# Optimization experiments

Measured on AMD Instinct MI355X. Metric: run time of the kernel, lower is better.

Reference implementation:

```python
import jax, jax.numpy as jnp
import numpy as np

X_DIM, R_DIM, U_DIM, V_DIM, H_DIM = 64, 64, 64, 64, 128


def setup_inputs() -> dict:
    key = jax.random.key(0)
    k1, k2, k3, k4, k5 = jax.random.split(key, 5)
    n, i, j = 8, 32, 32
    r = jax.random.normal(k1, (n, i, j, R_DIM), dtype=jnp.float32)
    u = jax.random.normal(k2, (n, R_DIM, U_DIM, V_DIM), dtype=jnp.float32)
    v = jax.random.normal(k3, (n, i, j, V_DIM), dtype=jnp.float32)
    # xavier_uniform scaling: gain=1, fan computed over last two dims per torch default
    def xavier(k, shape):
        fan_in, fan_out = shape[-1], shape[-2]
        # torch xavier on >2D tensor: fan_in = shape[1]*prod(shape[2:]), fan_out = shape[0]*prod(shape[2:])
        rf = int(np.prod(shape[2:])) if len(shape) > 2 else 1
        fi = shape[1] * rf
        fo = shape[0] * rf
        bound = float(np.sqrt(6.0 / (fi + fo)))
        return jax.random.uniform(k, shape, dtype=jnp.float32, minval=-bound, maxval=bound)
    w1 = xavier(k4, (R_DIM, U_DIM, V_DIM, H_DIM))
    w2 = xavier(k5, (X_DIM, R_DIM, H_DIM))
    return {"r": r, "u": u, "v": v, "w1": w1, "w2": w2}


def reference(r, u, v, w1, w2):
    # contract w1 with u over (u_dim, v_dim) -> per-batch tensor a[n, r, v', h]
    # original: einsum('ruvh,nruv,nijv->nijrh')
    a = jnp.einsum('ruvh,nruv->nrvh', w1, u)          # contract u axis; v survives? no:
    # Careful: in 'ruvh,nruv,nijv->nijrh', v is contracted across all three.
    # Do it in two GEMM-friendly steps: first contract u-axis, keeping v.
    # a: [n, r, v, h] (contracted only over u)
    a = jnp.einsum('ruvh,nruv->nrvh', w1, u)
    # then contract v with v-tensor: [n,i,j,v] x [n,r,v,h] -> [n,i,j,r,h]
    x = jax.nn.relu(jnp.einsum('nijv,nrvh->nijrh', v, a))
    # second einsum: 'xrh,nijr,nijrh->nijx'
    # fuse r-weighting into x first (elementwise over r), then contract (r,h) with w2
    out = jnp.einsum('xrh,nijrh->nijx', w2, x * r[..., None])
    return out
```

## Files before the change

### kernel.cpp

```cpp
#include <hip/hip_runtime.h>
#include <hip/hip_bf16.h>

#define RD 64
#define UD 64
#define VD 64
#define HD 128
#define XD 64
#define NB 8
#define SITES 1024

typedef float f32x4 __attribute__((ext_vector_type(4)));
typedef float f32x2 __attribute__((ext_vector_type(2)));
typedef __bf16 bf16x4 __attribute__((ext_vector_type(4)));
typedef __bf16 bf16x8 __attribute__((ext_vector_type(8)));
typedef unsigned int u32x4 __attribute__((ext_vector_type(4)));
typedef unsigned short u16;
typedef unsigned short u16x4 __attribute__((ext_vector_type(4)));

__device__ __forceinline__ void lds_barrier() {
  __builtin_amdgcn_s_waitcnt(0xC07F);
  __builtin_amdgcn_s_barrier();
}

__global__ void kprep(const float* __restrict__ w2, u16* __restrict__ w2t,
                      const float* __restrict__ r, float* __restrict__ rt,
                      const float* __restrict__ u, float* __restrict__ ut) {
  __shared__ float tl[64][68];
  int b = blockIdx.x;
  int t = threadIdx.x;
  if (b < 256) {
    int rr = b >> 2, qq = b & 3;
    for (int i = 0; i < 8; ++i) {
      int idx = qq * 2048 + i * 256 + t;
      int x = idx >> 7, h = idx & 127;
      float val = w2[((size_t)x * RD + rr) * HD + h];
      __hip_bfloat16 hv = __float2bfloat16(val);
      w2t[((size_t)rr * XD + x) * HD + h] = *(u16*)&hv;
    }
  } else if (b < 384) {
    int bb = b - 256;
    int n = bb >> 4, sb = (bb & 15) * 64;
    for (int i = 0; i < 4; ++i) {
      int flat = i * 256 + t;
      int s = flat >> 4, ch = flat & 15;
      f32x4 d = *(const f32x4*)(r + ((size_t)(n * SITES + sb + s) * RD + ch * 4));
      *(f32x4*)&tl[s][ch * 4] = d;
    }
    __syncthreads();
    for (int i = 0; i < 4; ++i) {
      int flat = i * 256 + t;
      int rr = flat >> 4, ch = flat & 15;
      f32x4 o;
      o.x = tl[ch * 4 + 0][rr];
      o.y = tl[ch * 4 + 1][rr];
      o.z = tl[ch * 4 + 2][rr];
      o.w = tl[ch * 4 + 3][rr];
      *(f32x4*)(rt + ((size_t)(n * RD + rr) * SITES + sb + ch * 4)) = o;
    }
  } else {
    int f = (b - 384) * 256 + t;
    int nh = f & 1, v = (f >> 1) & 63, uu = (f >> 7) & 63, rr = f >> 13;
    f32x4 o;
#pragma unroll
    for (int k = 0; k < 4; ++k)
      o[k] = u[(((size_t)(nh * 4 + k) * RD + rr) * UD + uu) * VD + v];
    *(f32x4*)(ut + (size_t)f * 4) = o;
  }
}

#define PF 8
__global__ __launch_bounds__(256, 1) void k_a_full(const float* __restrict__ w1,
                                                   const float* __restrict__ ut,
                                                   u16* __restrict__ at) {
  __shared__ float tile[8 * 128 * 17];
  int b = blockIdx.x;
  int rr = b >> 2, vq = b & 3;
  int t = threadIdx.x;
  int vl = t >> 4;
  int hs = t & 15;
  int v = vq * 16 + vl;
  int h0 = hs * 8;
  const float* w1p = w1 + ((size_t)rr * UD * VD + v) * HD + h0;
  const float* up  = ut + ((size_t)rr * UD * VD + v) * NB;

  f32x4 accA[8], accB[8];
#pragma unroll
  for (int n = 0; n < 8; ++n) { accA[n] = (f32x4)0.f; accB[n] = (f32x4)0.f; }

  f32x4 wa[PF], wb[PF], ua[PF], ub[PF];
#pragma unroll
  for (int p = 0; p < PF; ++p) {
    wa[p] = *(const f32x4*)(w1p + (size_t)p * 8192);
    wb[p] = *(const f32x4*)(w1p + (size_t)p * 8192 + 4);
    ua[p] = *(const f32x4*)(up + (size_t)p * 512);
    ub[p] = *(const f32x4*)(up + (size_t)p * 512 + 4);
  }

#define KA_CONSUME(P)                                                     \
  {                                                                       \
    f32x4 w0 = wa[P], w1v = wb[P], u0 = ua[P], u1 = ub[P];                \
    accA[0] += w0 * u0.x; accB[0] += w1v * u0.x;                          \
    accA[1] += w0 * u0.y; accB[1] += w1v * u0.y;                          \
    accA[2] += w0 * u0.z; accB[2] += w1v * u0.z;                          \
    accA[3] += w0 * u0.w; accB[3] += w1v * u0.w;                          \
    accA[4] += w0 * u1.x; accB[4] += w1v * u1.x;                          \
    accA[5] += w0 * u1.y; accB[5] += w1v * u1.y;                          \
    accA[6] += w0 * u1.z; accB[6] += w1v * u1.z;                          \
    accA[7] += w0 * u1.w; accB[7] += w1v * u1.w;                          \
  }

#pragma unroll 8
  for (int uu = 0; uu < 56; ++uu) {
    const int p = uu & 7;
    f32x4 w0 = wa[p], w1v = wb[p], u0 = ua[p], u1 = ub[p];
    wa[p] = *(const f32x4*)(w1p + (size_t)(uu + 8) * 8192);
    wb[p] = *(const f32x4*)(w1p + (size_t)(uu + 8) * 8192 + 4);
    ua[p] = *(const f32x4*)(up + (size_t)(uu + 8) * 512);
    ub[p] = *(const f32x4*)(up + (size_t)(uu + 8) * 512 + 4);
    accA[0] += w0 * u0.x; accB[0] += w1v * u0.x;
    accA[1] += w0 * u0.y; accB[1] += w1v * u0.y;
    accA[2] += w0 * u0.z; accB[2] += w1v * u0.z;
    accA[3] += w0 * u0.w; accB[3] += w1v * u0.w;
    accA[4] += w0 * u1.x; accB[4] += w1v * u1.x;
    accA[5] += w0 * u1.y; accB[5] += w1v * u1.y;
    accA[6] += w0 * u1.z; accB[6] += w1v * u1.z;
    accA[7] += w0 * u1.w; accB[7] += w1v * u1.w;
  }
  KA_CONSUME(0) KA_CONSUME(1) KA_CONSUME(2) KA_CONSUME(3)
  KA_CONSUME(4) KA_CONSUME(5) KA_CONSUME(6) KA_CONSUME(7)
#undef KA_CONSUME

#pragma unroll
  for (int n = 0; n < 8; ++n)
#pragma unroll
    for (int j = 0; j < 4; ++j) {
      tile[((n << 7) + h0 + j) * 17 + vl] = accA[n][j];
      tile[((n << 7) + h0 + 4 + j) * 17 + vl] = accB[n][j];
    }
  __syncthreads();

#pragma unroll
  for (int k = 0; k < 16; ++k) {
    int flat = k * 256 + t;
    int c4 = flat & 3, h = (flat >> 2) & 127, n = flat >> 9;
    const float* src = &tile[((n << 7) + h) * 17 + c4 * 4];
    u16x4 o;
#pragma unroll
    for (int j = 0; j < 4; ++j) {
      __hip_bfloat16 hv = __float2bfloat16(src[j]);
      o[j] = *(u16*)&hv;
    }
    *(u16x4*)(at + (((size_t)n * RD + rr) * HD + h) * VD + vq * 16 + c4 * 4) = o;
  }
}

__global__ __launch_bounds__(256, 1) void k_main(const float* __restrict__ vin,
                                                 const u16* __restrict__ at,
                                                 const u16* __restrict__ w2t,
                                                 const float* __restrict__ rt,
                                                 float* __restrict__ pbuf) {
  __shared__ __align__(16) char Plds[2 * 128 * 256];
  int b = blockIdx.x;
  int rc = b & 7, st = (b >> 3) & 7, n = b >> 6;
  int t = threadIdx.x;
  int w = t >> 6, L = t & 63, q = L >> 4, c = L & 15;
  int g2m = w >> 1, g2x = w & 1;

  bf16x8 vf[4][2];
#pragma unroll
  for (int nt = 0; nt < 4; ++nt)
#pragma unroll
    for (int ks = 0; ks < 2; ++ks) {
      int s = (w & 1) * 64 + nt * 16 + c;
      const float* vp = vin + ((size_t)(n * SITES + st * 128 + s) * VD + ks * 32 + q * 8);
      f32x4 a0 = *(const f32x4*)vp;
      f32x4 a1 = *(const f32x4*)(vp + 4);
      bf16x8 f;
      f[0] = (__bf16)a0.x; f[1] = (__bf16)a0.y; f[2] = (__bf16)a0.z; f[3] = (__bf16)a0.w;
      f[4] = (__bf16)a1.x; f[5] = (__bf16)a1.y; f[6] = (__bf16)a1.z; f[7] = (__bf16)a1.w;
      vf[nt][ks] = f;
    }

  f32x4 o[4][2];
#pragma unroll
  for (int i = 0; i < 4; i++)
#pragma unroll
    for (int j = 0; j < 2; j++) o[i][j] = (f32x4)0.f;

  int g1m = w >> 1, g1n = w & 1;
  for (int rr = rc * 8; rr < rc * 8 + 8; ++rr) {
    const u16* abase = at + (size_t)(n * RD + rr) * 8192;

    bf16x8 af[4][2];
#pragma unroll
    for (int mt = 0; mt < 4; ++mt)
#pragma unroll
      for (int ks = 0; ks < 2; ++ks) {
        int h = g1m * 64 + mt * 16 + c;
        int vb = ks * 4 + q;
        af[mt][ks] = *(const bf16x8*)(abase + (size_t)h * VD + vb * 8);
      }
    u32x4 wraw[2][4];
#pragma unroll
    for (int xt = 0; xt < 2; ++xt)
#pragma unroll
      for (int k2 = 0; k2 < 4; ++k2) {
        int xg = g2x * 32 + xt * 16 + c;
        wraw[xt][k2] = *(const u32x4*)((const char*)w2t +
                        (((size_t)(rr * XD + xg)) * HD + k2 * 32 + q * 8) * 2);
      }
    float rsc[4];
#pragma unroll
    for (int nt = 0; nt < 4; ++nt)
      rsc[nt] = rt[(size_t)(n * RD + rr) * SITES + st * 128 + g1n * 64 + nt * 16 + c];

    f32x4 cc[4][4];
#pragma unroll
    for (int mt = 0; mt < 4; ++mt)
#pragma unroll
      for (int nt = 0; nt < 4; ++nt) cc[mt][nt] = (f32x4)0.f;
#pragma unroll
    for (int ks = 0; ks < 2; ++ks)
#pragma unroll
      for (int mt = 0; mt < 4; ++mt)
#pragma unroll
        for (int nt = 0; nt < 4; ++nt)
          cc[mt][nt] = __builtin_amdgcn_mfma_f32_16x16x32_bf16(af[mt][ks], vf[nt][ks],
                                                               cc[mt][nt], 0, 0, 0);

    char* PB = Plds + (rr & 1) * 32768;
#pragma unroll
    for (int mt = 0; mt < 4; ++mt)
#pragma unroll
      for (int nt = 0; nt < 4; ++nt) {
        float sc = rsc[nt];
        bf16x4 pv;
#pragma unroll
        for (int jj = 0; jj < 4; ++jj) {
          float x = cc[mt][nt][jj];
          x = x > 0.f ? x : 0.f;
          pv[jj] = (__bf16)(x * sc);
        }
        int s = g1n * 64 + nt * 16 + c;
        int blk = g1m * 8 + mt * 2 + (q >> 1);
        *(bf16x4*)(PB + (size_t)s * 256 + (size_t)((blk ^ c) * 16 + (q & 1) * 8)) = pv;
      }
    lds_barrier();

#pragma unroll
    for (int k2 = 0; k2 < 4; ++k2) {
      bf16x8 wf0 = __builtin_bit_cast(bf16x8, wraw[0][k2]);
      bf16x8 wf1 = __builtin_bit_cast(bf16x8, wraw[1][k2]);
#pragma unroll
      for (int mt = 0; mt < 4; ++mt) {
        int s = g2m * 64 + mt * 16 + c;
        int blk = k2 * 4 + q;
        bf16x8 pf = *(const bf16x8*)(PB + (size_t)s * 256 + (size_t)((blk ^ c) * 16));
        o[mt][0] = __builtin_amdgcn_mfma_f32_16x16x32_bf16(pf, wf0, o[mt][0], 0, 0, 0);
        o[mt][1] = __builtin_amdgcn_mfma_f32_16x16x32_bf16(pf, wf1, o[mt][1], 0, 0, 0);
      }
    }
  }
#pragma unroll
  for (int mt = 0; mt < 4; ++mt)
#pragma unroll
    for (int xt = 0; xt < 2; ++xt) {
      int s0 = g2m * 64 + mt * 16 + q * 4;
      int x = g2x * 32 + xt * 16 + c;
      size_t off = ((((size_t)rc * NB + n) * 8 + st) * XD + x) * 128 + s0;
      *(f32x4*)(pbuf + off) = o[mt][xt];
    }
}

__global__ __launch_bounds__(256) void k_reduce(const float* __restrict__ pbuf,
                                                float* __restrict__ out) {
  __shared__ float tile[128][17];
  int b = blockIdx.x;
  int n = b >> 5, st = (b >> 2) & 7, xq = b & 3;
  int t = threadIdx.x;
  int sq = t & 31, xl = t >> 5;
#pragma unroll
  for (int p = 0; p < 2; ++p) {
    int x = xq * 16 + p * 8 + xl;
    f32x4 sum = (f32x4)0.f;
#pragma unroll
    for (int rcc = 0; rcc < 8; ++rcc) {
      size_t off = ((((size_t)rcc * NB + n) * 8 + st) * XD + x) * 128 + sq * 4;
      f32x4 d = *(const f32x4*)(pbuf + off);
      sum.x += d.x; sum.y += d.y; sum.z += d.z; sum.w += d.w;
    }
#pragma unroll
    for (int k = 0; k < 4; ++k) tile[sq * 4 + k][p * 8 + xl] = sum[k];
  }
  __syncthreads();
#pragma unroll
  for (int k = 0; k < 2; ++k) {
    int flat = k * 256 + t;
    int s = flat >> 2, c4 = flat & 3;
    f32x4 o;
#pragma unroll
    for (int j = 0; j < 4; ++j) o[j] = tile[s][c4 * 4 + j];
    *(f32x4*)(out + ((size_t)(n * SITES + st * 128 + s) * XD + xq * 16 + c4 * 4)) = o;
  }
}

extern "C" void kernel_launch(void* const* d_in, const int* in_sizes, int n_in,
                              void* d_out, int out_size, void* d_ws, size_t ws_size,
                              hipStream_t stream) {
  const float* r  = (const float*)d_in[0];
  const float* u  = (const float*)d_in[1];
  const float* v  = (const float*)d_in[2];
  const float* w1 = (const float*)d_in[3];
  const float* w2 = (const float*)d_in[4];
  float* out = (float*)d_out;
  char* ws = (char*)d_ws;
  u16* at     = (u16*)(ws);
  u16* w2t    = (u16*)(ws + ((size_t)8 << 20));
  float* rt   = (float*)(ws + ((size_t)9 << 20));
  float* ut   = (float*)(ws + ((size_t)11 << 20));
  float* pbuf = (float*)(ws + ((size_t)19 << 20));

  hipLaunchKernelGGL(kprep, dim3(2432), dim3(256), 0, stream, w2, w2t, r, rt, u, ut);
  hipLaunchKernelGGL(k_a_full, dim3(256), dim3(256), 0, stream, w1, ut, at);
  hipLaunchKernelGGL(k_main, dim3(512), dim3(256), 0, stream, v, at, w2t, rt, pbuf);
  hipLaunchKernelGGL(k_reduce, dim3(256), dim3(256), 0, stream, pbuf, out);
}
```

Measured before the change: 259.6 us.

## Stage w1/u slabs into LDS via async global_load_lds double buffering

Replaces the register-prefetch pipeline in the w1×u contraction kernel with a double-buffered LDS staging scheme. Chunks of 8 u-rows of the w1 and ut slabs are copied directly into shared memory with global_load_lds while the previous chunk is consumed from LDS. The aim is more memory-level parallelism and less VGPR pressure than the 8-deep register prefetch. The cost is extra LDS traffic, a larger shared allocation, and a barrier per chunk. It also relies on the barrier covering the async loads, which the code does not make explicit.

After: 261.7 us. No clear change (+0.8%).

```diff
diff --git a/kernel.cpp b/kernel.cpp
--- a/kernel.cpp
+++ b/kernel.cpp
@@ -21,6 +21,11 @@
   __builtin_amdgcn_s_waitcnt(0xC07F);
   __builtin_amdgcn_s_barrier();
 }
+
+#define GLOAD_LDS(g, l)                                                   \
+  __builtin_amdgcn_global_load_lds(                                       \
+      (const __attribute__((address_space(1))) void*)(g),                 \
+      (__attribute__((address_space(3))) void*)(l), 16, 0, 0)
 
 __global__ void kprep(const float* __restrict__ w2, u16* __restrict__ w2t,
                       const float* __restrict__ r, float* __restrict__ rt,
@@ -68,68 +73,72 @@
   }
 }
 
-#define PF 8
 __global__ __launch_bounds__(256, 1) void k_a_full(const float* __restrict__ w1,
                                                    const float* __restrict__ ut,
                                                    u16* __restrict__ at) {
-  __shared__ float tile[8 * 128 * 17];
+  __shared__ __align__(16) float smem[34816];
   int b = blockIdx.x;
   int rr = b >> 2, vq = b & 3;
   int t = threadIdx.x;
+  int w = t >> 6, L = t & 63;
   int vl = t >> 4;
   int hs = t & 15;
-  int v = vq * 16 + vl;
   int h0 = hs * 8;
-  const float* w1p = w1 + ((size_t)rr * UD * VD + v) * HD + h0;
-  const float* up  = ut + ((size_t)rr * UD * VD + v) * NB;
+
+  const float* w1slab = w1 + (size_t)rr * UD * VD * HD + (size_t)vq * 16 * HD;
+  const float* utslab = ut + (size_t)rr * UD * VD * NB + (size_t)vq * 16 * NB;
 
   f32x4 accA[8], accB[8];
 #pragma unroll
   for (int n = 0; n < 8; ++n) { accA[n] = (f32x4)0.f; accB[n] = (f32x4)0.f; }
 
-  f32x4 wa[PF], wb[PF], ua[PF], ub[PF];
-#pragma unroll
-  for (int p = 0; p < PF; ++p) {
-    wa[p] = *(const f32x4*)(w1p + (size_t)p * 8192);
-    wb[p] = *(const f32x4*)(w1p + (size_t)p * 8192 + 4);
-    ua[p] = *(const f32x4*)(up + (size_t)p * 512);
-    ub[p] = *(const f32x4*)(up + (size_t)p * 512 + 4);
-  }
-
-#define KA_CONSUME(P)                                                     \
-  {                                                                       \
-    f32x4 w0 = wa[P], w1v = wb[P], u0 = ua[P], u1 = ub[P];                \
-    accA[0] += w0 * u0.x; accB[0] += w1v * u0.x;                          \
-    accA[1] += w0 * u0.y; accB[1] += w1v * u0.y;                          \
-    accA[2] += w0 * u0.z; accB[2] += w1v * u0.z;                          \
-    accA[3] += w0 * u0.w; accB[3] += w1v * u0.w;                          \
-    accA[4] += w0 * u1.x; accB[4] += w1v * u1.x;                          \
-    accA[5] += w0 * u1.y; accB[5] += w1v * u1.y;                          \
-    accA[6] += w0 * u1.z; accB[6] += w1v * u1.z;                          \
-    accA[7] += w0 * u1.w; accB[7] += w1v * u1.w;                          \
-  }
-
-#pragma unroll 8
-  for (int uu = 0; uu < 56; ++uu) {
-    const int p = uu & 7;
-    f32x4 w0 = wa[p], w1v = wb[p], u0 = ua[p], u1 = ub[p];
-    wa[p] = *(const f32x4*)(w1p + (size_t)(uu + 8) * 8192);
-    wb[p] = *(const f32x4*)(w1p + (size_t)(uu + 8) * 8192 + 4);
-    ua[p] = *(const f32x4*)(up + (size_t)(uu + 8) * 512);
-    ub[p] = *(const f32x4*)(up + (size_t)(uu + 8) * 512 + 4);
-    accA[0] += w0 * u0.x; accB[0] += w1v * u0.x;
-    accA[1] += w0 * u0.y; accB[1] += w1v * u0.y;
-    accA[2] += w0 * u0.z; accB[2] += w1v * u0.z;
-    accA[3] += w0 * u0.w; accB[3] += w1v * u0.w;
-    accA[4] += w0 * u1.x; accB[4] += w1v * u1.x;
-    accA[5] += w0 * u1.y; accB[5] += w1v * u1.y;
-    accA[6] += w0 * u1.z; accB[6] += w1v * u1.z;
-    accA[7] += w0 * u1.w; accB[7] += w1v * u1.w;
-  }
-  KA_CONSUME(0) KA_CONSUME(1) KA_CONSUME(2) KA_CONSUME(3)
-  KA_CONSUME(4) KA_CONSUME(5) KA_CONSUME(6) KA_CONSUME(7)
-#undef KA_CONSUME
-
+#define STAGE(CC, SEL)                                                        \
+  {                                                                           \
+    float* wb = smem + (SEL)*16384;                                           \
+    float* ub = smem + 32768 + (SEL)*1024;                                    \
+    const float* wsrc = w1slab + (size_t)(CC)*8 * 8192;                       \
+    const float* usrc = utslab + (size_t)(CC)*8 * 512;                        \
+    _Pragma("unroll")                                                         \
+    for (int i = 0; i < 16; ++i) {                                            \
+      int s = w * 1024 + i * 64 + L;    \
+      GLOAD_LDS(wsrc + (size_t)(s >> 9) * 8192 + (size_t)(s & 511) * 4,       \
+                wb + (size_t)(w * 1024 + i * 64) * 4);                        \
+    }                                                                         \
+    {                                                                         \
+      int s2 = w * 64 + L;                        \
+      GLOAD_LDS(usrc + (size_t)(s2 >> 5) * 512 + (size_t)(s2 & 31) * 4,       \
+                ub + (size_t)(w * 64) * 4);                                   \
+    }                                                                         \
+  }
+
+  STAGE(0, 0)
+  __syncthreads();
+  int sel = 0;
+  for (int cc = 0; cc < 8; ++cc) {
+    if (cc < 7) STAGE(cc + 1, sel ^ 1)
+    const float* wb = smem + sel * 16384;
+    const float* ub = smem + 32768 + sel * 1024;
+#pragma unroll
+    for (int uul = 0; uul < 8; ++uul) {
+      f32x4 w0  = *(const f32x4*)(wb + uul * 2048 + vl * 128 + h0);
+      f32x4 w1v = *(const f32x4*)(wb + uul * 2048 + vl * 128 + h0 + 4);
+      f32x4 u0  = *(const f32x4*)(ub + uul * 128 + vl * 8);
+      f32x4 u1  = *(const f32x4*)(ub + uul * 128 + vl * 8 + 4);
+      accA[0] += w0 * u0.x; accB[0] += w1v * u0.x;
+      accA[1] += w0 * u0.y; accB[1] += w1v * u0.y;
+      accA[2] += w0 * u0.z; accB[2] += w1v * u0.z;
+      accA[3] += w0 * u0.w; accB[3] += w1v * u0.w;
+      accA[4] += w0 * u1.x; accB[4] += w1v * u1.x;
+      accA[5] += w0 * u1.y; accB[5] += w1v * u1.y;
+      accA[6] += w0 * u1.z; accB[6] += w1v * u1.z;
+      accA[7] += w0 * u1.w; accB[7] += w1v * u1.w;
+    }
+    __syncthreads();
+    sel ^= 1;
+  }
+#undef STAGE
+
+  float* tile = smem;
 #pragma unroll
   for (int n = 0; n < 8; ++n)
 #pragma unroll
```
